# Kernel optimization log

Measured on AMD Instinct MI355X. Metric: run time of the kernel, lower is better.

## Reference

```python
import jax, jax.numpy as jnp
import numpy as np

N = 50000
E = 800000
F_IN = 256
C = 64  # embedding_size, heads=1
EDGE_DIM = 2
NEG_SLOPE = 0.01


def setup_inputs() -> dict:
    key = jax.random.key(0)
    ks = jax.random.split(key, 12)
    s = 1.0 / np.sqrt(C)
    return {
        "x": jax.random.normal(ks[0], (N, F_IN), jnp.float32),
        "edge_index": jax.random.randint(ks[1], (2, E), 0, N, jnp.int64),
        "edge_attr": jax.random.normal(ks[2], (E, EDGE_DIM), jnp.float32),
        "Wf": jax.random.normal(ks[3], (F_IN, C), jnp.float32) / np.sqrt(F_IN),
        "bf": jnp.zeros((C,), jnp.float32),
        "Wq": jax.random.normal(ks[4], (C, C), jnp.float32) * s,
        "bq": jnp.zeros((C,), jnp.float32),
        "Wk": jax.random.normal(ks[5], (C, C), jnp.float32) * s,
        "bk": jnp.zeros((C,), jnp.float32),
        "Wv": jax.random.normal(ks[6], (C, C), jnp.float32) * s,
        "bv": jnp.zeros((C,), jnp.float32),
        "We": jax.random.normal(ks[7], (EDGE_DIM, C), jnp.float32) / np.sqrt(EDGE_DIM),
        "Wskip": jax.random.normal(ks[8], (C, C), jnp.float32) * s,
        "bskip": jnp.zeros((C,), jnp.float32),
    }


def reference(x, edge_index, edge_attr, Wf, bf, Wq, bq, Wk, bk, Wv, bv, We, Wskip, bskip):
    n = x.shape[0]
    src, dst = edge_index[0], edge_index[1]
    inv_sqrt_c = 1.0 / np.sqrt(C)

    h = jax.nn.leaky_relu(x @ Wf + bf, NEG_SLOPE)
    e = edge_attr @ We  # [E, C] edge embedding (lin_edge, no bias), same each layer

    for _ in range(3):
        q = h @ Wq + bq
        k = h @ Wk + bk
        v = h @ Wv + bv
        kj = k[src] + e                                  # [E, C] key + edge feat
        alpha = jnp.sum(q[dst] * kj, axis=-1) * inv_sqrt_c  # [E]
        # per-destination softmax
        m = jax.ops.segment_max(alpha, dst, num_segments=n)
        ex = jnp.exp(alpha - m[dst])
        den = jax.ops.segment_sum(ex, dst, num_segments=n)
        a = ex / den[dst]                                # [E]
        msg = (v[src] + e) * a[:, None]                  # [E, C]
        agg = jax.ops.segment_sum(msg, dst, num_segments=n)  # [N, C]
        h = jax.nn.leaky_relu(agg + h @ Wskip + bskip, NEG_SLOPE)  # root_weight skip
    return h
```

## Files before the change

kernel.cpp:

```cpp
#include <hip/hip_runtime.h>
#include <hip/hip_fp16.h>

#define NN 50000
#define NE 800000
#define FIN 256
#define C 64
#define NEG_SLOPE 0.01f
#define SCAN_BLOCKS ((NN + 255) / 256)

typedef float f32x16 __attribute__((ext_vector_type(16)));

__device__ __forceinline__ float leaky(float v) { return v > 0.f ? v : NEG_SLOPE * v; }

__device__ __forceinline__ float wave_sum(float x) {
    int v = __float_as_int(x);
#define DPP_ADD(ctrl) \
    x += __int_as_float(__builtin_amdgcn_update_dpp(0, v, ctrl, 0xF, 0xF, false)); \
    v = __float_as_int(x);
    DPP_ADD(0x111)
    DPP_ADD(0x112)
    DPP_ADD(0x114)
    DPP_ADD(0x118)
    DPP_ADD(0x142)
    DPP_ADD(0x143)
#undef DPP_ADD
    return __int_as_float(__builtin_amdgcn_readlane(v, 63));
}

__global__ __launch_bounds__(256) void k_tw(const float* __restrict__ Wq,
                                            const float* __restrict__ Wk,
                                            const float* __restrict__ Wv,
                                            const float* __restrict__ Ws,
                                            float* __restrict__ Wt) {
    const int idx = blockIdx.x * 256 + threadIdx.x;
    if (idx >= 4 * 64 * 64) return;
    const int m = idx >> 12, r = idx & 4095, c = r >> 6, k = r & 63;
    const float* W = (m == 0) ? Wq : (m == 1) ? Wk : (m == 2) ? Wv : Ws;
    Wt[idx] = W[k * 64 + c];
}

#define FEAT_NPB 16

__global__ __launch_bounds__(256) void k_feat(const float* __restrict__ x,
                                              const float* __restrict__ Wf,
                                              const float* __restrict__ bf,
                                              float* __restrict__ h) {
    __shared__ float4 Sx[FEAT_NPB][64];
    __shared__ float part[FEAT_NPB][4][64];
    const int t = threadIdx.x;
    const int lane = t & 63;
    const int w = __builtin_amdgcn_readfirstlane(t) >> 6;
    const int base = blockIdx.x * FEAT_NPB;

    const float4* x4 = (const float4*)x;
#pragma unroll
    for (int i = 0; i < 4; ++i) {
        const int idx = t + i * 256;
        const int row = idx >> 6, c4 = idx & 63;
        Sx[row][c4] = x4[(size_t)(base + row) * 64 + c4];
    }

    float wrk[64];
#pragma unroll
    for (int k = 0; k < 64; ++k)
        wrk[k] = Wf[(size_t)(w * 64 + k) * 64 + lane];

    __syncthreads();

#pragma unroll
    for (int i = 0; i < FEAT_NPB; ++i) {
        float a0 = 0.f, a1 = 0.f, a2 = 0.f, a3 = 0.f;
#pragma unroll
        for (int j = 0; j < 16; ++j) {
            const float4 xv = Sx[i][w * 16 + j];
            a0 = fmaf(xv.x, wrk[4 * j + 0], a0);
            a1 = fmaf(xv.y, wrk[4 * j + 1], a1);
            a2 = fmaf(xv.z, wrk[4 * j + 2], a2);
            a3 = fmaf(xv.w, wrk[4 * j + 3], a3);
        }
        part[i][w][lane] = (a0 + a1) + (a2 + a3);
    }
    __syncthreads();

#pragma unroll
    for (int j = 0; j < 4; ++j) {
        const int o = t + j * 256;
        const int node = o >> 6, col = o & 63;
        const float r = part[node][0][col] + part[node][1][col]
                      + part[node][2][col] + part[node][3][col] + bf[col];
        h[(size_t)(base + node) * 64 + col] = leaky(r);
    }
}

#define QKVS_NPB 32

__global__ __launch_bounds__(256) void k_qkvs(const float* __restrict__ h,
                                              const float* __restrict__ Wt,
                                              const float* __restrict__ bq,
                                              const float* __restrict__ bk,
                                              const float* __restrict__ bv,
                                              const float* __restrict__ bs,
                                              float* __restrict__ qkvs) {
    const int t = threadIdx.x;
    const int lane = t & 63;
    const int sec = __builtin_amdgcn_readfirstlane(t) >> 6;
    const int base = blockIdx.x * QKVS_NPB;

    int m, cidx;
    float bias;
    if (sec == 0)      { m = 0; cidx = lane; bias = bq[lane]; }
    else if (sec == 1) { m = 3; cidx = lane; bias = bs[lane]; }
    else {
        cidx = ((sec - 2) << 5) + (lane >> 1);
        m = 1 + (lane & 1);
        bias = (lane & 1) ? bv[cidx] : bk[cidx];
    }

    const float4* wb = (const float4*)(Wt + ((size_t)m << 12) + ((size_t)cidx << 6));
    float4 w[16];
#pragma unroll
    for (int j = 0; j < 16; ++j) w[j] = wb[j];

    const int nmax = (base + QKVS_NPB <= NN) ? QKVS_NPB : (NN - base);
    for (int i = 0; i < nmax; ++i) {
        const float* hrow = h + (size_t)(base + i) * 64;
        f32x16 ha, hb, hc, hd;
        asm volatile("s_load_dwordx16 %0, %4, 0x0\n\t"
                     "s_load_dwordx16 %1, %4, 0x40\n\t"
                     "s_load_dwordx16 %2, %4, 0x80\n\t"
                     "s_load_dwordx16 %3, %4, 0xc0\n\t"
                     "s_waitcnt lgkmcnt(0)"
                     : "=&s"(ha), "=&s"(hb), "=&s"(hc), "=&s"(hd)
                     : "s"(hrow));
        float a0 = 0.f, a1 = 0.f, a2 = 0.f, a3 = 0.f;
#pragma unroll
        for (int j = 0; j < 4; ++j) {
            a0 = fmaf(ha[4 * j + 0], w[j].x, a0);
            a1 = fmaf(ha[4 * j + 1], w[j].y, a1);
            a2 = fmaf(ha[4 * j + 2], w[j].z, a2);
            a3 = fmaf(ha[4 * j + 3], w[j].w, a3);
        }
#pragma unroll
        for (int j = 0; j < 4; ++j) {
            a0 = fmaf(hb[4 * j + 0], w[4 + j].x, a0);
            a1 = fmaf(hb[4 * j + 1], w[4 + j].y, a1);
            a2 = fmaf(hb[4 * j + 2], w[4 + j].z, a2);
            a3 = fmaf(hb[4 * j + 3], w[4 + j].w, a3);
        }
#pragma unroll
        for (int j = 0; j < 4; ++j) {
            a0 = fmaf(hc[4 * j + 0], w[8 + j].x, a0);
            a1 = fmaf(hc[4 * j + 1], w[8 + j].y, a1);
            a2 = fmaf(hc[4 * j + 2], w[8 + j].z, a2);
            a3 = fmaf(hc[4 * j + 3], w[8 + j].w, a3);
        }
#pragma unroll
        for (int j = 0; j < 4; ++j) {
            a0 = fmaf(hd[4 * j + 0], w[12 + j].x, a0);
            a1 = fmaf(hd[4 * j + 1], w[12 + j].y, a1);
            a2 = fmaf(hd[4 * j + 2], w[12 + j].z, a2);
            a3 = fmaf(hd[4 * j + 3], w[12 + j].w, a3);
        }
        const float val = ((a0 + a1) + (a2 + a3)) + bias;
        float* orow = qkvs + (size_t)(base + i) * 192;
        if (sec == 0) {
            orow[lane] = val;
        } else if (sec == 1) {
            orow[128 + lane] = val;
        } else {
            __half* kvh = (__half*)(orow + 64);
            kvh[((sec - 2) << 6) + lane] = __float2half(val);
        }
    }
}

__global__ __launch_bounds__(256) void k_hist(const int* __restrict__ ei,
                                              int* __restrict__ deg) {
    const int e = blockIdx.x * 256 + threadIdx.x;
    if (e >= NE) return;
    atomicAdd(&deg[ei[NE + e]], 1);
}

__global__ __launch_bounds__(256) void k_blocksum(const int* __restrict__ deg,
                                                  int* __restrict__ bsum) {
    __shared__ int sh[256];
    const int t = threadIdx.x;
    const int idx = blockIdx.x * 256 + t;
    sh[t] = (idx < NN) ? deg[idx] : 0;
    __syncthreads();
#pragma unroll
    for (int off = 128; off > 0; off >>= 1) {
        if (t < off) sh[t] += sh[t + off];
        __syncthreads();
    }
    if (t == 0) bsum[blockIdx.x] = sh[0];
}

__global__ __launch_bounds__(256) void k_scanb(const int* __restrict__ bsum,
                                               int* __restrict__ boff) {
    __shared__ int sh[256];
    const int t = threadIdx.x;
    const int v = (t < SCAN_BLOCKS) ? bsum[t] : 0;
    sh[t] = v;
    __syncthreads();
#pragma unroll
    for (int off = 1; off < 256; off <<= 1) {
        const int x = (t >= off) ? sh[t - off] : 0;
        __syncthreads();
        sh[t] += x;
        __syncthreads();
    }
    if (t < SCAN_BLOCKS) boff[t] = sh[t] - v;
}

__global__ __launch_bounds__(256) void k_writeptr(const int* __restrict__ deg,
                                                  const int* __restrict__ boff,
                                                  int* __restrict__ row_ptr,
                                                  int* __restrict__ cursor) {
    __shared__ int sh[256];
    const int t = threadIdx.x;
    const int idx = blockIdx.x * 256 + t;
    const int v = (idx < NN) ? deg[idx] : 0;
    sh[t] = v;
    __syncthreads();
#pragma unroll
    for (int off = 1; off < 256; off <<= 1) {
        const int x = (t >= off) ? sh[t - off] : 0;
        __syncthreads();
        sh[t] += x;
        __syncthreads();
    }
    if (idx < NN) {
        const int r = boff[blockIdx.x] + sh[t] - v;
        row_ptr[idx] = r;
        cursor[idx] = r;
    }
    if (idx == 0) row_ptr[NN] = NE;
}

__global__ __launch_bounds__(256) void k_csr(const int* __restrict__ ei,
                                             const float* __restrict__ eattr,
                                             int* __restrict__ cursor,
                                             float4* __restrict__ erec) {
    const int e = blockIdx.x * 256 + threadIdx.x;
    if (e >= NE) return;
    const int dst = ei[NE + e];
    const int pos = atomicAdd(&cursor[dst], 1);
    erec[pos] = make_float4(__int_as_float(ei[e]), eattr[e * 2], eattr[e * 2 + 1], 0.f);
}

__global__ __launch_bounds__(256) void k_conv(const int* __restrict__ row_ptr,
                                              const float4* __restrict__ erec,
                                              const float* __restrict__ We,
                                              const float* __restrict__ qkvs,
                                              float* __restrict__ hout) {
    const int lane = threadIdx.x & 63;
    const int wv = __builtin_amdgcn_readfirstlane(threadIdx.x) >> 6;
    const int d = blockIdx.x * 4 + wv;
    if (d >= NN) return;
    const float we0 = We[lane], we1 = We[C + lane];
    const float* qrow = qkvs + (size_t)d * 192;
    const float q = qrow[lane];
    const float g0 = wave_sum(q * we0);
    const float g1 = wave_sum(q * we1);
    const int i0 = row_ptr[d], i1 = row_ptr[d + 1];

    float m = -INFINITY, l = 0.f, acc = 0.f, S1 = 0.f, S2 = 0.f;
    int i = i0;
    for (; i + 3 < i1; i += 4) {
        const float4 r0 = erec[i], r1 = erec[i + 1], r2 = erec[i + 2], r3 = erec[i + 3];
        const __half2* b0 = (const __half2*)(qkvs + (size_t)__float_as_int(r0.x) * 192 + 64);
        const __half2* b1 = (const __half2*)(qkvs + (size_t)__float_as_int(r1.x) * 192 + 64);
        const __half2* b2 = (const __half2*)(qkvs + (size_t)__float_as_int(r2.x) * 192 + 64);
        const __half2* b3 = (const __half2*)(qkvs + (size_t)__float_as_int(r3.x) * 192 + 64);
        const __half2 kv0 = b0[lane], kv1 = b1[lane], kv2 = b2[lane], kv3 = b3[lane];
        const float kf0 = __low2float(kv0), vf0 = __high2float(kv0);
        const float kf1 = __low2float(kv1), vf1 = __high2float(kv1);
        const float kf2 = __low2float(kv2), vf2 = __high2float(kv2);
        const float kf3 = __low2float(kv3), vf3 = __high2float(kv3);
        const float P0 = (wave_sum(q * kf0) + g0 * r0.y + g1 * r0.z) * 0.125f;
        const float P1 = (wave_sum(q * kf1) + g0 * r1.y + g1 * r1.z) * 0.125f;
        const float P2 = (wave_sum(q * kf2) + g0 * r2.y + g1 * r2.z) * 0.125f;
        const float P3 = (wave_sum(q * kf3) + g0 * r3.y + g1 * r3.z) * 0.125f;
        const float mn = fmaxf(fmaxf(m, fmaxf(P0, P1)), fmaxf(P2, P3));
        const float s = __expf(m - mn);
        const float e0 = __expf(P0 - mn), e1 = __expf(P1 - mn);
        const float e2 = __expf(P2 - mn), e3 = __expf(P3 - mn);
        l = l * s + ((e0 + e1) + (e2 + e3));
        acc = acc * s + vf0 * e0 + vf1 * e1 + vf2 * e2 + vf3 * e3;
        S1 = S1 * s + r0.y * e0 + r1.y * e1 + r2.y * e2 + r3.y * e3;
        S2 = S2 * s + r0.z * e0 + r1.z * e1 + r2.z * e2 + r3.z * e3;
        m = mn;
    }
    for (; i < i1; ++i) {
        const float4 r0 = erec[i];
        const __half2* b0 = (const __half2*)(qkvs + (size_t)__float_as_int(r0.x) * 192 + 64);
        const __half2 kv0 = b0[lane];
        const float kf0 = __low2float(kv0), vf0 = __high2float(kv0);
        const float P0 = (wave_sum(q * kf0) + g0 * r0.y + g1 * r0.z) * 0.125f;
        const float mn = fmaxf(m, P0);
        const float s = __expf(m - mn);
        const float e0 = __expf(P0 - mn);
        l = l * s + e0;
        acc = acc * s + vf0 * e0;
        S1 = S1 * s + r0.y * e0;
        S2 = S2 * s + r0.z * e0;
        m = mn;
    }
    const float res = (l > 0.f) ? (acc + S1 * we0 + S2 * we1) / l : 0.f;
    hout[(size_t)d * C + lane] = leaky(res + qrow[128 + lane]);
}

extern "C" void kernel_launch(void* const* d_in, const int* in_sizes, int n_in,
                              void* d_out, int out_size, void* d_ws, size_t ws_size,
                              hipStream_t stream) {
    const float* x     = (const float*)d_in[0];
    const int*   ei    = (const int*)d_in[1];
    const float* eattr = (const float*)d_in[2];
    const float* Wf    = (const float*)d_in[3];
    const float* bf    = (const float*)d_in[4];
    const float* Wq    = (const float*)d_in[5];
    const float* bq    = (const float*)d_in[6];
    const float* Wk    = (const float*)d_in[7];
    const float* bk    = (const float*)d_in[8];
    const float* Wv    = (const float*)d_in[9];
    const float* bv    = (const float*)d_in[10];
    const float* We    = (const float*)d_in[11];
    const float* Ws    = (const float*)d_in[12];
    const float* bs    = (const float*)d_in[13];
    float* out = (float*)d_out;

    char* p = (char*)d_ws;
    float*  h       = (float*)p;  p += (size_t)NN * C * 4;
    float*  qkvs    = (float*)p;  p += (size_t)NN * 192 * 4;
    float*  Wt      = (float*)p;  p += (size_t)4 * 64 * 64 * 4;
    int*    deg     = (int*)p;    p += (size_t)NN * 4;
    int*    row_ptr = (int*)p;    p += (size_t)(NN + 1) * 4;
    int*    cursor  = (int*)p;    p += (size_t)NN * 4;
    int*    bsum    = (int*)p;    p += (size_t)SCAN_BLOCKS * 4;
    int*    boff    = (int*)p;    p += (size_t)SCAN_BLOCKS * 4;
    float4* erec    = (float4*)p; p += (size_t)NE * 16;

    k_tw<<<64, 256, 0, stream>>>(Wq, Wk, Wv, Ws, Wt);
    hipMemsetAsync(deg, 0, (size_t)NN * 4, stream);
    k_hist<<<(NE + 255) / 256, 256, 0, stream>>>(ei, deg);
    k_blocksum<<<SCAN_BLOCKS, 256, 0, stream>>>(deg, bsum);
    k_scanb<<<1, 256, 0, stream>>>(bsum, boff);
    k_writeptr<<<SCAN_BLOCKS, 256, 0, stream>>>(deg, boff, row_ptr, cursor);
    k_csr<<<(NE + 255) / 256, 256, 0, stream>>>(ei, eattr, cursor, erec);

    const int feat_grid = NN / FEAT_NPB;
    const int qkvs_grid = (NN + QKVS_NPB - 1) / QKVS_NPB;

    k_feat<<<feat_grid, 256, 0, stream>>>(x, Wf, bf, h);

    for (int layer = 0; layer < 3; ++layer) {
        k_qkvs<<<qkvs_grid, 256, 0, stream>>>(h, Wt, bq, bk, bv, bs, qkvs);
        float* hout = (layer == 2) ? out : h;
        k_conv<<<(NN + 3) / 4, 256, 0, stream>>>(row_ptr, erec, We, qkvs, hout);
    }
}
```

Before: 499.1 us.

## Split each wave into four 16-lane edge groups and pack edge records to 8 bytes

```diff
diff --git a/kernel.cpp b/kernel.cpp
--- a/kernel.cpp
+++ b/kernel.cpp
@@ -11,21 +11,6 @@
 typedef float f32x16 __attribute__((ext_vector_type(16)));
 
 __device__ __forceinline__ float leaky(float v) { return v > 0.f ? v : NEG_SLOPE * v; }
-
-__device__ __forceinline__ float wave_sum(float x) {
-    int v = __float_as_int(x);
-#define DPP_ADD(ctrl) \
-    x += __int_as_float(__builtin_amdgcn_update_dpp(0, v, ctrl, 0xF, 0xF, false)); \
-    v = __float_as_int(x);
-    DPP_ADD(0x111)
-    DPP_ADD(0x112)
-    DPP_ADD(0x114)
-    DPP_ADD(0x118)
-    DPP_ADD(0x142)
-    DPP_ADD(0x143)
-#undef DPP_ADD
-    return __int_as_float(__builtin_amdgcn_readlane(v, 63));
-}
 
 __global__ __launch_bounds__(256) void k_tw(const float* __restrict__ Wq,
                                             const float* __restrict__ Wk,
@@ -241,74 +226,111 @@
 __global__ __launch_bounds__(256) void k_csr(const int* __restrict__ ei,
                                              const float* __restrict__ eattr,
                                              int* __restrict__ cursor,
-                                             float4* __restrict__ erec) {
+                                             uint2* __restrict__ erec) {
     const int e = blockIdx.x * 256 + threadIdx.x;
     if (e >= NE) return;
     const int dst = ei[NE + e];
     const int pos = atomicAdd(&cursor[dst], 1);
-    erec[pos] = make_float4(__int_as_float(ei[e]), eattr[e * 2], eattr[e * 2 + 1], 0.f);
+    const __half2 a = __floats2half2_rn(eattr[e * 2], eattr[e * 2 + 1]);
+    erec[pos] = make_uint2((unsigned)ei[e], *(const unsigned*)&a);
 }
 
 __global__ __launch_bounds__(256) void k_conv(const int* __restrict__ row_ptr,
-                                              const float4* __restrict__ erec,
+                                              const uint2* __restrict__ erec,
                                               const float* __restrict__ We,
                                               const float* __restrict__ qkvs,
                                               float* __restrict__ hout) {
-    const int lane = threadIdx.x & 63;
-    const int wv = __builtin_amdgcn_readfirstlane(threadIdx.x) >> 6;
+    const int t = threadIdx.x;
+    const int lane = t & 63;
+    const int g = lane >> 4;
+    const int p = lane & 15;
+    const int wv = __builtin_amdgcn_readfirstlane(t) >> 6;
     const int d = blockIdx.x * 4 + wv;
     if (d >= NN) return;
-    const float we0 = We[lane], we1 = We[C + lane];
+
     const float* qrow = qkvs + (size_t)d * 192;
-    const float q = qrow[lane];
-    const float g0 = wave_sum(q * we0);
-    const float g1 = wave_sum(q * we1);
+    const float4 q4  = *(const float4*)(qrow + 4 * p);
+    const float4 w0  = *(const float4*)(We + 4 * p);
+    const float4 w1  = *(const float4*)(We + 64 + 4 * p);
+
+    float pg0 = q4.x * w0.x + q4.y * w0.y + q4.z * w0.z + q4.w * w0.w;
+    float pg1 = q4.x * w1.x + q4.y * w1.y + q4.z * w1.z + q4.w * w1.w;
+#pragma unroll
+    for (int mask = 1; mask <= 8; mask <<= 1) {
+        pg0 += __shfl_xor(pg0, mask);
+        pg1 += __shfl_xor(pg1, mask);
+    }
+    const float g0 = pg0, g1 = pg1;
+
     const int i0 = row_ptr[d], i1 = row_ptr[d + 1];
-
-    float m = -INFINITY, l = 0.f, acc = 0.f, S1 = 0.f, S2 = 0.f;
-    int i = i0;
-    for (; i + 3 < i1; i += 4) {
-        const float4 r0 = erec[i], r1 = erec[i + 1], r2 = erec[i + 2], r3 = erec[i + 3];
-        const __half2* b0 = (const __half2*)(qkvs + (size_t)__float_as_int(r0.x) * 192 + 64);
-        const __half2* b1 = (const __half2*)(qkvs + (size_t)__float_as_int(r1.x) * 192 + 64);
-        const __half2* b2 = (const __half2*)(qkvs + (size_t)__float_as_int(r2.x) * 192 + 64);
-        const __half2* b3 = (const __half2*)(qkvs + (size_t)__float_as_int(r3.x) * 192 + 64);
-        const __half2 kv0 = b0[lane], kv1 = b1[lane], kv2 = b2[lane], kv3 = b3[lane];
-        const float kf0 = __low2float(kv0), vf0 = __high2float(kv0);
-        const float kf1 = __low2float(kv1), vf1 = __high2float(kv1);
-        const float kf2 = __low2float(kv2), vf2 = __high2float(kv2);
-        const float kf3 = __low2float(kv3), vf3 = __high2float(kv3);
-        const float P0 = (wave_sum(q * kf0) + g0 * r0.y + g1 * r0.z) * 0.125f;
-        const float P1 = (wave_sum(q * kf1) + g0 * r1.y + g1 * r1.z) * 0.125f;
-        const float P2 = (wave_sum(q * kf2) + g0 * r2.y + g1 * r2.z) * 0.125f;
-        const float P3 = (wave_sum(q * kf3) + g0 * r3.y + g1 * r3.z) * 0.125f;
-        const float mn = fmaxf(fmaxf(m, fmaxf(P0, P1)), fmaxf(P2, P3));
+    const char* kvbase = (const char*)qkvs + 256 + ((size_t)p << 4);
+
+    float m = -1e30f, l = 0.f, S1 = 0.f, S2 = 0.f;
+    float4 acc = make_float4(0.f, 0.f, 0.f, 0.f);
+
+#pragma unroll 2
+    for (int i = i0 + g; i < i1; i += 4) {
+        const uint2 r = erec[i];
+        const __half2 ah = *(const __half2*)&r.y;
+        const float a0 = __low2float(ah), a1 = __high2float(ah);
+        const float4 kvl = *(const float4*)(kvbase + (size_t)r.x * 768);
+        const __half2* hv = (const __half2*)&kvl;
+        const float kf0 = __low2float(hv[0]), vf0 = __high2float(hv[0]);
+        const float kf1 = __low2float(hv[1]), vf1 = __high2float(hv[1]);
+        const float kf2 = __low2float(hv[2]), vf2 = __high2float(hv[2]);
+        const float kf3 = __low2float(hv[3]), vf3 = __high2float(hv[3]);
+        float dot = q4.x * kf0 + q4.y * kf1 + q4.z * kf2 + q4.w * kf3;
+        dot += __shfl_xor(dot, 1);
+        dot += __shfl_xor(dot, 2);
+        dot += __shfl_xor(dot, 4);
+        dot += __shfl_xor(dot, 8);
+        const float P = (dot + g0 * a0 + g1 * a1) * 0.125f;
+        const float mn = fmaxf(m, P);
         const float s = __expf(m - mn);
-        const float e0 = __expf(P0 - mn), e1 = __expf(P1 - mn);
-        const float e2 = __expf(P2 - mn), e3 = __expf(P3 - mn);
-        l = l * s + ((e0 + e1) + (e2 + e3));
-        acc = acc * s + vf0 * e0 + vf1 * e1 + vf2 * e2 + vf3 * e3;
-        S1 = S1 * s + r0.y * e0 + r1.y * e1 + r2.y * e2 + r3.y * e3;
-        S2 = S2 * s + r0.z * e0 + r1.z * e1 + r2.z * e2 + r3.z * e3;
+        const float e = __expf(P - mn);
+        l = l * s + e;
+        acc.x = acc.x * s + vf0 * e;
+        acc.y = acc.y * s + vf1 * e;
+        acc.z = acc.z * s + vf2 * e;
+        acc.w = acc.w * s + vf3 * e;
+        S1 = S1 * s + a0 * e;
+        S2 = S2 * s + a1 * e;
         m = mn;
     }
-    for (; i < i1; ++i) {
-        const float4 r0 = erec[i];
-        const __half2* b0 = (const __half2*)(qkvs + (size_t)__float_as_int(r0.x) * 192 + 64);
-        const __half2 kv0 = b0[lane];
-        const float kf0 = __low2float(kv0), vf0 = __high2float(kv0);
-        const float P0 = (wave_sum(q * kf0) + g0 * r0.y + g1 * r0.z) * 0.125f;
-        const float mn = fmaxf(m, P0);
-        const float s = __expf(m - mn);
-        const float e0 = __expf(P0 - mn);
-        l = l * s + e0;
-        acc = acc * s + vf0 * e0;
-        S1 = S1 * s + r0.y * e0;
-        S2 = S2 * s + r0.z * e0;
+
+#pragma unroll
+    for (int mask = 16; mask <= 32; mask <<= 1) {
+        const float mo  = __shfl_xor(m, mask);
+        const float lo  = __shfl_xor(l, mask);
+        const float axo = __shfl_xor(acc.x, mask);
+        const float ayo = __shfl_xor(acc.y, mask);
+        const float azo = __shfl_xor(acc.z, mask);
+        const float awo = __shfl_xor(acc.w, mask);
+        const float S1o = __shfl_xor(S1, mask);
+        const float S2o = __shfl_xor(S2, mask);
+        const float mn = fmaxf(m, mo);
+        const float sA = __expf(m - mn);
+        const float sB = __expf(mo - mn);
+        l     = l * sA + lo * sB;
+        acc.x = acc.x * sA + axo * sB;
+        acc.y = acc.y * sA + ayo * sB;
+        acc.z = acc.z * sA + azo * sB;
+        acc.w = acc.w * sA + awo * sB;
+        S1    = S1 * sA + S1o * sB;
+        S2    = S2 * sA + S2o * sB;
         m = mn;
     }
-    const float res = (l > 0.f) ? (acc + S1 * we0 + S2 * we1) / l : 0.f;
-    hout[(size_t)d * C + lane] = leaky(res + qrow[128 + lane]);
+
+    if (lane < 16) {
+        const float inv = (l > 0.f) ? 1.f / l : 0.f;
+        const float4 sk = *(const float4*)(qrow + 128 + 4 * p);
+        float4 r;
+        r.x = leaky((acc.x + S1 * w0.x + S2 * w1.x) * inv + sk.x);
+        r.y = leaky((acc.y + S1 * w0.y + S2 * w1.y) * inv + sk.y);
+        r.z = leaky((acc.z + S1 * w0.z + S2 * w1.z) * inv + sk.z);
+        r.w = leaky((acc.w + S1 * w0.w + S2 * w1.w) * inv + sk.w);
+        *(float4*)(hout + (size_t)d * C + 4 * p) = r;
+    }
 }
 
 extern "C" void kernel_launch(void* const* d_in, const int* in_sizes, int n_in,
@@ -339,7 +361,7 @@
     int*    cursor  = (int*)p;    p += (size_t)NN * 4;
     int*    bsum    = (int*)p;    p += (size_t)SCAN_BLOCKS * 4;
     int*    boff    = (int*)p;    p += (size_t)SCAN_BLOCKS * 4;
-    float4* erec    = (float4*)p; p += (size_t)NE * 16;
+    uint2*  erec    = (uint2*)p;  p += (size_t)NE * 8;
 
     k_tw<<<64, 256, 0, stream>>>(Wq, Wk, Wv, Ws, Wt);
     hipMemsetAsync(deg, 0, (size_t)NN * 4, stream);
```

Measured after the change: 497.2 us. Within noise of the previous version (-0.4%).
